# Performance work log

Measured on AMD Instinct MI355X. Metric: run time of the kernel, lower is better.

## Reference

```python
import jax, jax.numpy as jnp
import numpy as np

B, T, V, WD = 32, 2048, 50000, 300        # batch, max_doc_len, batch vocab, word_dim
P, L, ND = 150, 7, 2                      # total patterns, max_pattern_length, num_diags
BIAS_SCALE = 1.0
ZERO = -100.0                             # max-plus semiring zero (repo: neg_infinity = -100*ones)
# end state per pattern = pattern_length - 1, for pattern_specs {5:50, 6:50, 7:50}
END_STATES = np.concatenate([np.full(50, 4), np.full(50, 5), np.full(50, 6)]).astype(np.int32)


def setup_inputs() -> dict:
    key = jax.random.key(0)
    ks = jax.random.split(key, 10)
    diags = jax.random.normal(ks[0], (P * ND * L, WD), jnp.float32)
    diags = diags / jnp.linalg.norm(diags, axis=1, keepdims=True)  # normalize() in __init__
    return {
        "embeddings_matrix": jax.random.normal(ks[1], (WD, V), jnp.float32),
        "diags": diags,
        "bias": jax.random.normal(ks[2], (P * ND * L, 1), jnp.float32),
        "epsilon": jax.random.normal(ks[3], (P, L - 1), jnp.float32),
        "mlp_w0": jax.random.normal(ks[4], (P, 100), jnp.float32) * 0.1,
        "mlp_b0": jnp.zeros((100,), jnp.float32),
        "mlp_w1": jax.random.normal(ks[5], (100, 2), jnp.float32) * 0.1,
        "mlp_b1": jnp.zeros((2,), jnp.float32),
        "docs": jax.random.randint(ks[6], (B, T), 0, V),
        "doc_lens": jax.random.randint(ks[7], (B,), 5, T + 1),
    }


def reference(embeddings_matrix, diags, bias, epsilon, mlp_w0, mlp_b0, mlp_w1, mlp_b1, docs, doc_lens):
    # Max-plus semiring: from_float = identity, times = +, plus = max, one = 0, zero = -100.
    # Transition scores for every token in the batch vocabulary: [V, P*ND*L]
    trans = (diags @ embeddings_matrix + BIAS_SCALE * bias).T
    # Gather per doc token, reshape, time-major: [T, B, P, ND, L]
    tm = trans[docs].reshape(B, T, P, ND, L).transpose(1, 0, 2, 3, 4)

    end_states = jnp.asarray(END_STATES)               # [P]
    active = jnp.arange(T)[:, None] < doc_lens[None, :]  # [T, B]

    zero_pad = jnp.full((B, P, 1), ZERO, trans.dtype)
    restart_pad = jnp.zeros((B, P, 1), trans.dtype)      # semiring one
    hid0 = jnp.full((B, P, L), ZERO, trans.dtype).at[:, :, 0].set(0.0)
    scores0 = jnp.full((B, P), ZERO, trans.dtype)
    eps_val = epsilon                                    # epsilon_scale = semiring one (=0) -> identity

    def step(carry, xs):
        hid, sc = carry
        tmat, act = xs  # tmat: [B, P, ND, L], act: [B]
        # epsilon transitions (shift by one state, additive in max-plus)
        after_eps = jnp.maximum(hid, jnp.concatenate([zero_pad, hid[:, :, :-1] + eps_val], axis=2))
        # main-path transitions (diag index -1), with restart padding at state 0
        main = jnp.concatenate([restart_pad, after_eps[:, :, :-1] + tmat[:, :, -1, :-1]], axis=2)
        # self loops (diag index 0); self_loop_scale = semiring one = 0
        self_loop = hid + tmat[:, :, 0, :]
        hid = jnp.maximum(main, self_loop)
        end_vals = jnp.take_along_axis(hid, end_states[None, :, None], axis=2)[:, :, 0]  # [B, P]
        sc = jnp.where(act[:, None], jnp.maximum(sc, end_vals), sc)
        return (hid, sc), None

    (_, scores), _ = jax.lax.scan(step, (hid0, scores0), (tm, active))
    # MLP head: Linear -> relu -> Linear
    h = scores @ mlp_w0 + mlp_b0
    return jax.nn.relu(h) @ mlp_w1 + mlp_b1
```

## Files before the change

kernel.cpp:

```cpp
#include <hip/hip_runtime.h>
#include <stdint.h>

#define B_   32
#define T_   2048
#define V_   50000
#define WD_  300
#define P_   150
#define KP   320
#define MP   2112
#define MB2  2176
#define NPAD2 50176
#define VT_  391
#define MT_  17
#define NWG3 6664
#define NEGC (-1.0e30f)

#define WS_DIAGSB      32112640u
#define WS_TRANS_BIG   54067200u
#define WS_TRANS_SMALL 33505280u
#define WS_AUX_BIG     265267200u
#define WS_AUX_SMALL   244705280u
#define AUX_BYTES      864260u
#define WS_NEED_BIG    (WS_AUX_BIG + AUX_BYTES)
#define WS_NEED_SMALL  (WS_AUX_SMALL + AUX_BYTES)

typedef __attribute__((ext_vector_type(8))) short bf16x8;
typedef __attribute__((ext_vector_type(4))) float f32x4;

#define GLOAD_LDS16(gp, lp) __builtin_amdgcn_global_load_lds( \
    (__attribute__((address_space(1))) void*)(gp), \
    (__attribute__((address_space(3))) void*)(lp), 16, 0, 0)

__device__ __forceinline__ unsigned short f2bf(float f){
  unsigned u = __builtin_bit_cast(unsigned, f);
  u = u + 0x7fffu + ((u >> 16) & 1u);
  return (unsigned short)(u >> 16);
}
__device__ __forceinline__ float bf_lo(unsigned u){ return __builtin_bit_cast(float, u << 16); }
__device__ __forceinline__ float bf_hi(unsigned u){ return __builtin_bit_cast(float, u & 0xffff0000u); }

__global__ __launch_bounds__(256) void k_transpose_emb(const float* __restrict__ emb,
                                                       unsigned short* __restrict__ embT){
  __shared__ float tile[32][65];
  int v0 = blockIdx.x * 64, k0 = blockIdx.y * 32;
  int tid = threadIdx.x;
  #pragma unroll
  for (int it = 0; it < 8; ++it){
    int idx = it * 256 + tid;
    int kk = idx >> 6, vv = idx & 63;
    int k = k0 + kk, v = v0 + vv;
    float val = 0.f;
    if (k < WD_ && v < V_) val = emb[(size_t)k * V_ + v];
    tile[kk][vv] = val;
  }
  __syncthreads();
  int row = tid >> 2, c = tid & 3;
  unsigned short e[8];
  #pragma unroll
  for (int i = 0; i < 8; ++i) e[i] = f2bf(tile[c*8 + i][row]);
  uint4 pk;
  pk.x = (unsigned)e[0] | ((unsigned)e[1] << 16);
  pk.y = (unsigned)e[2] | ((unsigned)e[3] << 16);
  pk.z = (unsigned)e[4] | ((unsigned)e[5] << 16);
  pk.w = (unsigned)e[6] | ((unsigned)e[7] << 16);
  *(uint4*)&embT[(size_t)(v0 + row) * KP + k0 + c*8] = pk;
}

__global__ __launch_bounds__(256) void k_conv_diags(const float* __restrict__ diags,
                                                    unsigned short* __restrict__ diagsB){
  int gid = blockIdx.x * 256 + threadIdx.x;
  int m = gid / 80;
  int k4 = (gid % 80) * 4;
  unsigned short e[4];
  #pragma unroll
  for (int i = 0; i < 4; ++i){
    int k = k4 + i;
    float v = (m < 2100 && k < WD_) ? diags[m * WD_ + k] : 0.f;
    e[i] = f2bf(v);
  }
  uint2 pk;
  pk.x = (unsigned)e[0] | ((unsigned)e[1] << 16);
  pk.y = (unsigned)e[2] | ((unsigned)e[3] << 16);
  *(uint2*)&diagsB[(size_t)m * KP + k4] = pk;
}

__global__ __launch_bounds__(256) void k_zero(int* __restrict__ used, int* __restrict__ counter){
  int i = blockIdx.x * 256 + threadIdx.x;
  if (i < NPAD2) used[i] = 0;
  if (i == 0) *counter = 0;
}
__global__ __launch_bounds__(256) void k_mark(const int* __restrict__ docs,
                                              const int* __restrict__ dlens,
                                              int* __restrict__ used){
  int i = blockIdx.x * 256 + threadIdx.x;
  int b = i >> 11, t = i & 2047;
  if (t < dlens[b]) used[docs[i]] = 1;
}
__global__ __launch_bounds__(256) void k_compact(const int* __restrict__ used,
                                                 int* __restrict__ remap,
                                                 int* __restrict__ inv,
                                                 int* __restrict__ counter){
  int v = blockIdx.x * 256 + threadIdx.x;
  if (v >= V_) return;
  if (used[v]){
    int id = atomicAdd(counter, 1);
    remap[v] = id;
    inv[id] = v;
  }
}
__global__ __launch_bounds__(256) void k_docsC(const int* __restrict__ docs,
                                               const int* __restrict__ dlens,
                                               const int* __restrict__ remap,
                                               int* __restrict__ docsC){
  int i = blockIdx.x * 256 + threadIdx.x;
  int b = i >> 11, t = i & 2047;
  docsC[i] = (t < dlens[b]) ? remap[docs[i]] : 0;
}

__global__ __launch_bounds__(256, 4) void k_gemm(const unsigned short* __restrict__ embT,
                                                 const unsigned short* __restrict__ diagsB,
                                                 const float* __restrict__ bias,
                                                 const int* __restrict__ inv,
                                                 const int* __restrict__ nusedp,
                                                 unsigned short* __restrict__ trans){
  __shared__ char smem[33792];
  int nused = *nusedp;
  int orig = blockIdx.x;
  int xcd = orig & 7, idx0 = orig >> 3;
  int vt = (idx0 / MT_) * 8 + xcd;
  int mt = idx0 % MT_;
  int v0 = vt * 128, m0 = mt * 128;
  if (v0 >= nused) return;

  int tid = threadIdx.x;
  int w = tid >> 6, l = tid & 63;
  int wv = w & 1, wm = w >> 1;
  int lrow = l & 15, lq = l >> 4;

  int rA0 = tid >> 2, rA1 = 64 + (tid >> 2);
  size_t ga0 = (size_t)((v0 + rA0 < nused) ? inv[v0 + rA0] : 0) * KP;
  size_t ga1 = (size_t)((v0 + rA1 < nused) ? inv[v0 + rA1] : 0) * KP;

  f32x4 acc[4][4];
  #pragma unroll
  for (int i = 0; i < 4; ++i)
    #pragma unroll
    for (int j = 0; j < 4; ++j)
      acc[i][j] = (f32x4){0.f, 0.f, 0.f, 0.f};

  auto STAGE = [&](int buf, int kt){
    int k0 = kt * 32;
    char* bA = smem + buf * 16384;
    char* bB = bA + 8192;
    int slot = tid & 3;
    {
      int idx = tid;
      int sc = slot ^ ((rA0 >> 1) & 3);
      GLOAD_LDS16(&embT[ga0 + k0 + sc * 8], bA + idx * 16);
      int row = idx >> 2;
      int scB = slot ^ ((row >> 1) & 3);
      GLOAD_LDS16(&diagsB[(size_t)(m0 + row) * KP + k0 + scB * 8], bB + idx * 16);
    }
    {
      int idx = 256 + tid;
      int sc = slot ^ ((rA1 >> 1) & 3);
      GLOAD_LDS16(&embT[ga1 + k0 + sc * 8], bA + idx * 16);
      int row = idx >> 2;
      int scB = slot ^ ((row >> 1) & 3);
      GLOAD_LDS16(&diagsB[(size_t)(m0 + row) * KP + k0 + scB * 8], bB + idx * 16);
    }
  };

  STAGE(0, 0);
  #pragma unroll
  for (int kt = 0; kt < 10; ++kt){
    if (kt < 9){
      STAGE((kt + 1) & 1, kt + 1);
      asm volatile("s_waitcnt vmcnt(4)" ::: "memory");
    } else {
      asm volatile("s_waitcnt vmcnt(0)" ::: "memory");
    }
    __builtin_amdgcn_s_barrier();
    __builtin_amdgcn_sched_barrier(0);
    char* bA = smem + (kt & 1) * 16384;
    char* bB = bA + 8192;
    bf16x8 af[4], bg[4];
    #pragma unroll
    for (int i = 0; i < 4; ++i){
      int row = wv * 64 + i * 16 + lrow;
      af[i] = *(const bf16x8*)(bA + row * 64 + (lq ^ ((row >> 1) & 3)) * 16);
    }
    #pragma unroll
    for (int j = 0; j < 4; ++j){
      int row = wm * 64 + j * 16 + lrow;
      bg[j] = *(const bf16x8*)(bB + row * 64 + (lq ^ ((row >> 1) & 3)) * 16);
    }
    #pragma unroll
    for (int i = 0; i < 4; ++i)
      #pragma unroll
      for (int j = 0; j < 4; ++j)
        acc[i][j] = __builtin_amdgcn_mfma_f32_16x16x32_bf16(af[i], bg[j], acc[i][j], 0, 0, 0);
    __builtin_amdgcn_sched_barrier(0);
    __builtin_amdgcn_s_barrier();
  }

  float bv4[4];
  #pragma unroll
  for (int j = 0; j < 4; ++j){
    int mg = m0 + wm * 64 + j * 16 + lrow;
    bv4[j] = (mg < 2100) ? bias[mg] : 0.f;
  }
  unsigned short* eb = (unsigned short*)smem;
  #pragma unroll
  for (int i = 0; i < 4; ++i)
    #pragma unroll
    for (int j = 0; j < 4; ++j)
      #pragma unroll
      for (int r = 0; r < 4; ++r){
        int row = wv * 64 + i * 16 + lq * 4 + r;
        int col = wm * 64 + j * 16 + lrow;
        eb[row * 132 + col] = f2bf(acc[i][j][r] + bv4[j]);
      }
  __syncthreads();
  #pragma unroll
  for (int it = 0; it < 16; ++it){
    int idx2 = it * 256 + tid;
    int row = idx2 >> 5, chq = idx2 & 31;
    int vg = v0 + row, mg = m0 + chq * 4;
    if (vg < nused && mg < MP){
      uint2 val = *(const uint2*)(smem + row * 264 + chq * 8);
      *(uint2*)&trans[(size_t)vg * MP + mg] = val;
    }
  }
}

template<int CH>
__global__ __launch_bounds__(192) void k_scan(const unsigned short* __restrict__ trans,
                                              const int* __restrict__ docsC,
                                              const int* __restrict__ doc_lens,
                                              const float* __restrict__ epsilon,
                                              float* __restrict__ chunkout){
  constexpr int NCHT = T_ / CH;
  __shared__ int sdocs[CH];
  int b = blockIdx.x / NCHT, ch = blockIdx.x % NCHT;
  int doclen = doc_lens[b];
  int tbase = ch * CH;
  if (tbase >= doclen) return;
  int tid = threadIdx.x;
  if (tid < CH) sdocs[tid] = docsC[b * T_ + tbase + tid];
  __syncthreads();
  int p = tid;
  if (p >= P_) return;
  float eps_r[6];
  #pragma unroll
  for (int i = 0; i < 6; ++i) eps_r[i] = epsilon[p*6 + i];
  int endsel = p / 50;

  float col[7][7], bvec[7], uvec[7], w;
  #pragma unroll
  for (int j = 0; j < 7; ++j)
    #pragma unroll
    for (int l = 0; l < 7; ++l) col[j][l] = (j == l) ? 0.f : NEGC;
  #pragma unroll
  for (int l = 0; l < 7; ++l){ bvec[l] = NEGC; uvec[l] = NEGC; }
  w = NEGC;

  const char* transB = (const char*)trans;

  auto LOADQ = [&](unsigned* q, int s){
    int idx = s < CH - 1 ? s : CH - 1;
    const unsigned* rp = (const unsigned*)(transB + (size_t)sdocs[idx] * (MP*2) + p*28);
    #pragma unroll
    for (int i = 0; i < 7; ++i) q[i] = rp[i];
  };

  auto step = [&](const unsigned* q, bool act){
    float tsf[7], tmn[6];
    tsf[0]=bf_lo(q[0]); tsf[1]=bf_hi(q[0]);
    tsf[2]=bf_lo(q[1]); tsf[3]=bf_hi(q[1]);
    tsf[4]=bf_lo(q[2]); tsf[5]=bf_hi(q[2]);
    tsf[6]=bf_lo(q[3]); tmn[0]=bf_hi(q[3]);
    tmn[1]=bf_lo(q[4]); tmn[2]=bf_hi(q[4]);
    tmn[3]=bf_lo(q[5]); tmn[4]=bf_hi(q[5]);
    tmn[5]=bf_lo(q[6]);
    #pragma unroll
    for (int j = 0; j < 7; ++j){
      #pragma unroll
      for (int l = 6; l >= 1; --l){
        if (l < j) continue;
        if (l == j){ col[j][l] = col[j][l] + tsf[l]; continue; }
        float ae;
        if (l - 1 == j) ae = col[j][l-1];
        else ae = fmaxf(col[j][l-1], col[j][l-2] + eps_r[l-2]);
        col[j][l] = fmaxf(ae + tmn[l-1], col[j][l] + tsf[l]);
      }
      if (j == 0) col[0][0] += tsf[0];
    }
    #pragma unroll
    for (int l = 6; l >= 1; --l){
      float ae;
      if (l == 1) ae = fmaxf(bvec[0], -100.0f);
      else ae = fmaxf(bvec[l-1], bvec[l-2] + eps_r[l-2]);
      bvec[l] = fmaxf(ae + tmn[l-1], bvec[l] + tsf[l]);
    }
    bvec[0] = fmaxf(0.0f, bvec[0] + tsf[0]);
    if (act){
      #pragma unroll
      for (int j = 0; j < 7; ++j){
        float c4 = (j <= 4) ? col[j][4] : NEGC;
        float c5 = (j <= 5) ? col[j][5] : NEGC;
        float c6 = col[j][6];
        float ce = (endsel == 0) ? c4 : ((endsel == 1) ? c5 : c6);
        uvec[j] = fmaxf(uvec[j], ce);
      }
      float be = (endsel == 0) ? bvec[4] : ((endsel == 1) ? bvec[5] : bvec[6]);
      w = fmaxf(w, be);
    }
  };

  unsigned qa0[7], qa1[7], qa2[7], qa3[7];
  unsigned qb0[7], qb1[7], qb2[7], qb3[7];
  LOADQ(qa0, 0); LOADQ(qa1, 1); LOADQ(qa2, 2); LOADQ(qa3, 3);
  for (int s = 0; s < CH; s += 8){
    LOADQ(qb0, s + 4); LOADQ(qb1, s + 5); LOADQ(qb2, s + 6); LOADQ(qb3, s + 7);
    step(qa0, (tbase + s)     < doclen);
    step(qa1, (tbase + s + 1) < doclen);
    step(qa2, (tbase + s + 2) < doclen);
    step(qa3, (tbase + s + 3) < doclen);
    LOADQ(qa0, s + 8); LOADQ(qa1, s + 9); LOADQ(qa2, s + 10); LOADQ(qa3, s + 11);
    step(qb0, (tbase + s + 4) < doclen);
    step(qb1, (tbase + s + 5) < doclen);
    step(qb2, (tbase + s + 6) < doclen);
    step(qb3, (tbase + s + 7) < doclen);
  }

  float out[44];
  int idx = 0;
  #pragma unroll
  for (int j = 0; j < 7; ++j)
    #pragma unroll
    for (int l = j; l < 7; ++l) out[idx++] = col[j][l];
  #pragma unroll
  for (int l = 0; l < 7; ++l) out[28 + l] = bvec[l];
  #pragma unroll
  for (int l = 0; l < 7; ++l) out[35 + l] = uvec[l];
  out[42] = w; out[43] = 0.f;
  float* dst = chunkout + ((size_t)(b * NCHT + ch) * P_ + p) * 44;
  #pragma unroll
  for (int i = 0; i < 11; ++i){
    float4 t2 = make_float4(out[4*i], out[4*i+1], out[4*i+2], out[4*i+3]);
    ((float4*)dst)[i] = t2;
  }
}

__global__ __launch_bounds__(192) void k_combine_mlp(const float* __restrict__ chunkout,
                                                     const int* __restrict__ doc_lens,
                                                     const float* __restrict__ w0,
                                                     const float* __restrict__ b0,
                                                     const float* __restrict__ w1,
                                                     const float* __restrict__ b1,
                                                     float* __restrict__ out,
                                                     int nch, int chsz){
  __shared__ float ssc[P_];
  __shared__ float sh[100];
  int b = blockIdx.x, tid = threadIdx.x;
  if (tid < P_){
    int p = tid;
    int doclen = doc_lens[b];
    int nact = (doclen + chsz - 1) / chsz;
    if (nact > nch) nact = nch;
    float h[7] = {0.f, -100.f, -100.f, -100.f, -100.f, -100.f, -100.f};
    float sc = -100.f;
    for (int ch = 0; ch < nact; ++ch){
      const float* rec = chunkout + ((size_t)(b * nch + ch) * P_ + p) * 44;
      float r[44];
      #pragma unroll
      for (int i = 0; i < 11; ++i){
        float4 t = ((const float4*)rec)[i];
        r[4*i] = t.x; r[4*i+1] = t.y; r[4*i+2] = t.z; r[4*i+3] = t.w;
      }
      #pragma unroll
      for (int j = 0; j < 7; ++j) sc = fmaxf(sc, r[35 + j] + h[j]);
      sc = fmaxf(sc, r[42]);
      constexpr int off[7] = {0, 7, 13, 18, 22, 25, 27};
      float nh[7];
      #pragma unroll
      for (int l = 0; l < 7; ++l){
        float v = r[28 + l];
        #pragma unroll
        for (int j = 0; j < 7; ++j){
          if (j <= l) v = fmaxf(v, r[off[j] + (l - j)] + h[j]);
        }
        nh[l] = v;
      }
      #pragma unroll
      for (int l = 0; l < 7; ++l) h[l] = nh[l];
    }
    ssc[p] = sc;
  }
  __syncthreads();
  if (tid < 100){
    float a = b0[tid];
    for (int pp = 0; pp < P_; ++pp) a += ssc[pp] * w0[pp * 100 + tid];
    sh[tid] = fmaxf(a, 0.f);
  }
  __syncthreads();
  if (tid < 2){
    float o = b1[tid];
    for (int j = 0; j < 100; ++j) o += sh[j] * w1[j * 2 + tid];
    out[b * 2 + tid] = o;
  }
}

extern "C" void kernel_launch(void* const* d_in, const int* in_sizes, int n_in,
                              void* d_out, int out_size, void* d_ws, size_t ws_size,
                              hipStream_t stream){
  const float* emb   = (const float*)d_in[0];
  const float* diags = (const float*)d_in[1];
  const float* bias  = (const float*)d_in[2];
  const float* eps   = (const float*)d_in[3];
  const float* w0    = (const float*)d_in[4];
  const float* b0    = (const float*)d_in[5];
  const float* w1    = (const float*)d_in[6];
  const float* b1    = (const float*)d_in[7];
  const int* docs    = (const int*)d_in[8];
  const int* dlens   = (const int*)d_in[9];

  if (ws_size < (size_t)WS_NEED_SMALL) return;
  bool big = ws_size >= (size_t)WS_NEED_BIG;

  char* ws = (char*)d_ws;
  unsigned short* embT   = (unsigned short*)(ws);
  unsigned short* diagsB = (unsigned short*)(ws + WS_DIAGSB);
  unsigned short* trans  = (unsigned short*)(ws + (big ? WS_TRANS_BIG : WS_TRANS_SMALL));
  char* aux              = ws + (big ? WS_AUX_BIG : WS_AUX_SMALL);
  int* used    = (int*)(aux);
  int* remap   = (int*)(aux + 200704u);
  int* inv     = (int*)(aux + 401408u);
  int* docsC   = (int*)(aux + 602112u);
  int* counter = (int*)(aux + 864256u);
  float* chunkout = (float*)(ws);
  float* outp = (float*)d_out;

  k_transpose_emb<<<dim3(NPAD2/64, KP/32), 256, 0, stream>>>(emb, embT);
  k_conv_diags<<<(MB2*80 + 255)/256, 256, 0, stream>>>(diags, diagsB);
  k_zero<<<NPAD2/256, 256, 0, stream>>>(used, counter);
  k_mark<<<B_*T_/256, 256, 0, stream>>>(docs, dlens, used);
  k_compact<<<(V_ + 255)/256, 256, 0, stream>>>(used, remap, inv, counter);
  k_docsC<<<B_*T_/256, 256, 0, stream>>>(docs, dlens, remap, docsC);
  k_gemm<<<NWG3, 256, 0, stream>>>(embT, diagsB, bias, inv, counter, trans);
  if (big){
    k_scan<32><<<B_ * 64, 192, 0, stream>>>(trans, docsC, dlens, eps, chunkout);
    k_combine_mlp<<<B_, 192, 0, stream>>>(chunkout, dlens, w0, b0, w1, b1, outp, 64, 32);
  } else {
    k_scan<64><<<B_ * 32, 192, 0, stream>>>(trans, docsC, dlens, eps, chunkout);
    k_combine_mlp<<<B_, 192, 0, stream>>>(chunkout, dlens, w0, b0, w1, b1, outp, 32, 64);
  }
}
```

Before: 181.7 us.

## Split chunked scan state columns across two workgroups per chunk

Each chunk's scan is split into two workgroups. One tracks start-state columns 0-2 of the max-plus transfer matrix and the other tracks columns 3-6 plus the from-start vector, which doubles the grid and roughly halves per-thread register state and arithmetic. The aim is more occupancy and parallelism in the latency-bound scan. In exchange, both halves reload the same transition rows, and the output is written as scalar stores to disjoint fields instead of packed float4 stores.

```diff
diff --git a/kernel.cpp b/kernel.cpp
--- a/kernel.cpp
+++ b/kernel.cpp
@@ -234,38 +234,20 @@
   }
 }
 
-template<int CH>
-__global__ __launch_bounds__(192) void k_scan(const unsigned short* __restrict__ trans,
-                                              const int* __restrict__ docsC,
-                                              const int* __restrict__ doc_lens,
-                                              const float* __restrict__ epsilon,
-                                              float* __restrict__ chunkout){
-  constexpr int NCHT = T_ / CH;
-  __shared__ int sdocs[CH];
-  int b = blockIdx.x / NCHT, ch = blockIdx.x % NCHT;
-  int doclen = doc_lens[b];
-  int tbase = ch * CH;
-  if (tbase >= doclen) return;
-  int tid = threadIdx.x;
-  if (tid < CH) sdocs[tid] = docsC[b * T_ + tbase + tid];
-  __syncthreads();
-  int p = tid;
-  if (p >= P_) return;
-  float eps_r[6];
-  #pragma unroll
-  for (int i = 0; i < 6; ++i) eps_r[i] = epsilon[p*6 + i];
-  int endsel = p / 50;
-
+template<int CH, int J0, int J1, bool DOB>
+__device__ __forceinline__ void scan_body(const char* __restrict__ transB,
+                                          const int* __restrict__ sdocs,
+                                          int tbase, int doclen,
+                                          const float* eps_r, int endsel, int p,
+                                          float* __restrict__ dst){
   float col[7][7], bvec[7], uvec[7], w;
   #pragma unroll
-  for (int j = 0; j < 7; ++j)
+  for (int j = J0; j < J1; ++j)
     #pragma unroll
     for (int l = 0; l < 7; ++l) col[j][l] = (j == l) ? 0.f : NEGC;
   #pragma unroll
   for (int l = 0; l < 7; ++l){ bvec[l] = NEGC; uvec[l] = NEGC; }
   w = NEGC;
-
-  const char* transB = (const char*)trans;
 
   auto LOADQ = [&](unsigned* q, int s){
     int idx = s < CH - 1 ? s : CH - 1;
@@ -284,7 +266,7 @@
     tmn[3]=bf_lo(q[5]); tmn[4]=bf_hi(q[5]);
     tmn[5]=bf_lo(q[6]);
     #pragma unroll
-    for (int j = 0; j < 7; ++j){
+    for (int j = J0; j < J1; ++j){
       #pragma unroll
       for (int l = 6; l >= 1; --l){
         if (l < j) continue;
@@ -296,25 +278,29 @@
       }
       if (j == 0) col[0][0] += tsf[0];
     }
-    #pragma unroll
-    for (int l = 6; l >= 1; --l){
-      float ae;
-      if (l == 1) ae = fmaxf(bvec[0], -100.0f);
-      else ae = fmaxf(bvec[l-1], bvec[l-2] + eps_r[l-2]);
-      bvec[l] = fmaxf(ae + tmn[l-1], bvec[l] + tsf[l]);
-    }
-    bvec[0] = fmaxf(0.0f, bvec[0] + tsf[0]);
+    if constexpr (DOB){
+      #pragma unroll
+      for (int l = 6; l >= 1; --l){
+        float ae;
+        if (l == 1) ae = fmaxf(bvec[0], -100.0f);
+        else ae = fmaxf(bvec[l-1], bvec[l-2] + eps_r[l-2]);
+        bvec[l] = fmaxf(ae + tmn[l-1], bvec[l] + tsf[l]);
+      }
+      bvec[0] = fmaxf(0.0f, bvec[0] + tsf[0]);
+    }
     if (act){
       #pragma unroll
-      for (int j = 0; j < 7; ++j){
+      for (int j = J0; j < J1; ++j){
         float c4 = (j <= 4) ? col[j][4] : NEGC;
         float c5 = (j <= 5) ? col[j][5] : NEGC;
         float c6 = col[j][6];
         float ce = (endsel == 0) ? c4 : ((endsel == 1) ? c5 : c6);
         uvec[j] = fmaxf(uvec[j], ce);
       }
-      float be = (endsel == 0) ? bvec[4] : ((endsel == 1) ? bvec[5] : bvec[6]);
-      w = fmaxf(w, be);
+      if constexpr (DOB){
+        float be = (endsel == 0) ? bvec[4] : ((endsel == 1) ? bvec[5] : bvec[6]);
+        w = fmaxf(w, be);
+      }
     }
   };
 
@@ -334,23 +320,52 @@
     step(qb3, (tbase + s + 7) < doclen);
   }
 
-  float out[44];
-  int idx = 0;
-  #pragma unroll
-  for (int j = 0; j < 7; ++j)
-    #pragma unroll
-    for (int l = j; l < 7; ++l) out[idx++] = col[j][l];
-  #pragma unroll
-  for (int l = 0; l < 7; ++l) out[28 + l] = bvec[l];
-  #pragma unroll
-  for (int l = 0; l < 7; ++l) out[35 + l] = uvec[l];
-  out[42] = w; out[43] = 0.f;
+  constexpr int off[7] = {0, 7, 13, 18, 22, 25, 27};
+  #pragma unroll
+  for (int j = J0; j < J1; ++j)
+    #pragma unroll
+    for (int l = j; l < 7; ++l) dst[off[j] + (l - j)] = col[j][l];
+  if constexpr (DOB){
+    #pragma unroll
+    for (int l = 0; l < 7; ++l) dst[28 + l] = bvec[l];
+  }
+  #pragma unroll
+  for (int j = J0; j < J1; ++j) dst[35 + j] = uvec[j];
+  if constexpr (DOB) dst[42] = w;
+}
+
+template<int CH>
+__global__ __launch_bounds__(192) void k_scan(const unsigned short* __restrict__ trans,
+                                              const int* __restrict__ docsC,
+                                              const int* __restrict__ doc_lens,
+                                              const float* __restrict__ epsilon,
+                                              float* __restrict__ chunkout){
+  constexpr int NCHT = T_ / CH;
+  __shared__ int sdocs[CH];
+  int raw = blockIdx.x;
+  int part = raw & 1;
+  int cid = raw >> 1;
+  int b = cid / NCHT, ch = cid % NCHT;
+  int doclen = doc_lens[b];
+  int tbase = ch * CH;
+  if (tbase >= doclen) return;
+  int tid = threadIdx.x;
+  if (tid < CH) sdocs[tid] = docsC[b * T_ + tbase + tid];
+  __syncthreads();
+  int p = tid;
+  if (p >= P_) return;
+  float eps_r[6];
+  #pragma unroll
+  for (int i = 0; i < 6; ++i) eps_r[i] = epsilon[p*6 + i];
+  int endsel = p / 50;
+
+  const char* transB = (const char*)trans;
   float* dst = chunkout + ((size_t)(b * NCHT + ch) * P_ + p) * 44;
-  #pragma unroll
-  for (int i = 0; i < 11; ++i){
-    float4 t2 = make_float4(out[4*i], out[4*i+1], out[4*i+2], out[4*i+3]);
-    ((float4*)dst)[i] = t2;
-  }
+
+  if (part == 0)
+    scan_body<CH, 0, 3, false>(transB, sdocs, tbase, doclen, eps_r, endsel, p, dst);
+  else
+    scan_body<CH, 3, 7, true >(transB, sdocs, tbase, doclen, eps_r, endsel, p, dst);
 }
 
 __global__ __launch_bounds__(192) void k_combine_mlp(const float* __restrict__ chunkout,
@@ -450,10 +465,10 @@
   k_docsC<<<B_*T_/256, 256, 0, stream>>>(docs, dlens, remap, docsC);
   k_gemm<<<NWG3, 256, 0, stream>>>(embT, diagsB, bias, inv, counter, trans);
   if (big){
-    k_scan<32><<<B_ * 64, 192, 0, stream>>>(trans, docsC, dlens, eps, chunkout);
+    k_scan<32><<<B_ * 64 * 2, 192, 0, stream>>>(trans, docsC, dlens, eps, chunkout);
     k_combine_mlp<<<B_, 192, 0, stream>>>(chunkout, dlens, w0, b0, w1, b1, outp, 64, 32);
   } else {
-    k_scan<64><<<B_ * 32, 192, 0, stream>>>(trans, docsC, dlens, eps, chunkout);
+    k_scan<64><<<B_ * 32 * 2, 192, 0, stream>>>(trans, docsC, dlens, eps, chunkout);
     k_combine_mlp<<<B_, 192, 0, stream>>>(chunkout, dlens, w0, b0, w1, b1, outp, 32, 64);
   }
 }
```

New measurement: 195.9 us. +7.8%, slower.

## Stage gathered trans rows through double-buffered shared memory in scan kernel

Applied to the files above, without the earlier changes.

The scan kernel now loads whole 4224-byte trans rows for groups of four tokens with coalesced uint4 loads from all threads into registers. It writes them into a double-buffered shared-memory tile, and each pattern thread then reads its 28-byte slice from LDS. This replaces the per-thread strided 4-byte global loads with a register-prefetch pipeline, aiming to cut uncoalesced global traffic. In exchange it adds two block barriers per group, about 33KB of LDS, and idle threads beyond P that must stay alive to help with loads.

```diff
diff --git a/kernel.cpp b/kernel.cpp
--- a/kernel.cpp
+++ b/kernel.cpp
@@ -241,7 +241,9 @@
                                               const float* __restrict__ epsilon,
                                               float* __restrict__ chunkout){
   constexpr int NCHT = T_ / CH;
+  constexpr int NG = CH / 4;
   __shared__ int sdocs[CH];
+  __shared__ char rows[2][4][4224];
   int b = blockIdx.x / NCHT, ch = blockIdx.x % NCHT;
   int doclen = doc_lens[b];
   int tbase = ch * CH;
@@ -250,11 +252,14 @@
   if (tid < CH) sdocs[tid] = docsC[b * T_ + tbase + tid];
   __syncthreads();
   int p = tid;
-  if (p >= P_) return;
-  float eps_r[6];
-  #pragma unroll
-  for (int i = 0; i < 6; ++i) eps_r[i] = epsilon[p*6 + i];
-  int endsel = p / 50;
+  bool act_p = p < P_;
+  float eps_r[6] = {0,0,0,0,0,0};
+  int endsel = 0;
+  if (act_p){
+    #pragma unroll
+    for (int i = 0; i < 6; ++i) eps_r[i] = epsilon[p*6 + i];
+    endsel = p / 50;
+  }
 
   float col[7][7], bvec[7], uvec[7], w;
   #pragma unroll
@@ -267,14 +272,31 @@
 
   const char* transB = (const char*)trans;
 
-  auto LOADQ = [&](unsigned* q, int s){
-    int idx = s < CH - 1 ? s : CH - 1;
-    const unsigned* rp = (const unsigned*)(transB + (size_t)sdocs[idx] * (MP*2) + p*28);
-    #pragma unroll
-    for (int i = 0; i < 7; ++i) q[i] = rp[i];
+  uint4 rg[4][2];
+  #pragma unroll
+  for (int r = 0; r < 4; ++r){ rg[r][0] = make_uint4(0,0,0,0); rg[r][1] = make_uint4(0,0,0,0); }
+
+  auto LOADG = [&](int g){
+    #pragma unroll
+    for (int r = 0; r < 4; ++r){
+      const uint4* src = (const uint4*)(transB + (size_t)sdocs[g*4 + r] * (MP*2));
+      rg[r][0] = src[tid];
+      if (tid < 72) rg[r][1] = src[192 + tid];
+    }
   };
-
-  auto step = [&](const unsigned* q, bool act){
+  auto WRITEG = [&](int buf){
+    #pragma unroll
+    for (int r = 0; r < 4; ++r){
+      uint4* dst = (uint4*)rows[buf][r];
+      dst[tid] = rg[r][0];
+      if (tid < 72) dst[192 + tid] = rg[r][1];
+    }
+  };
+
+  auto stepL = [&](const char* rp, bool act){
+    unsigned q[7];
+    #pragma unroll
+    for (int i = 0; i < 7; ++i) q[i] = *(const unsigned*)(rp + 4*i);
     float tsf[7], tmn[6];
     tsf[0]=bf_lo(q[0]); tsf[1]=bf_hi(q[0]);
     tsf[2]=bf_lo(q[1]); tsf[3]=bf_hi(q[1]);
@@ -318,38 +340,37 @@
     }
   };
 
-  unsigned qa0[7], qa1[7], qa2[7], qa3[7];
-  unsigned qb0[7], qb1[7], qb2[7], qb3[7];
-  LOADQ(qa0, 0); LOADQ(qa1, 1); LOADQ(qa2, 2); LOADQ(qa3, 3);
-  for (int s = 0; s < CH; s += 8){
-    LOADQ(qb0, s + 4); LOADQ(qb1, s + 5); LOADQ(qb2, s + 6); LOADQ(qb3, s + 7);
-    step(qa0, (tbase + s)     < doclen);
-    step(qa1, (tbase + s + 1) < doclen);
-    step(qa2, (tbase + s + 2) < doclen);
-    step(qa3, (tbase + s + 3) < doclen);
-    LOADQ(qa0, s + 8); LOADQ(qa1, s + 9); LOADQ(qa2, s + 10); LOADQ(qa3, s + 11);
-    step(qb0, (tbase + s + 4) < doclen);
-    step(qb1, (tbase + s + 5) < doclen);
-    step(qb2, (tbase + s + 6) < doclen);
-    step(qb3, (tbase + s + 7) < doclen);
-  }
-
-  float out[44];
-  int idx = 0;
-  #pragma unroll
-  for (int j = 0; j < 7; ++j)
-    #pragma unroll
-    for (int l = j; l < 7; ++l) out[idx++] = col[j][l];
-  #pragma unroll
-  for (int l = 0; l < 7; ++l) out[28 + l] = bvec[l];
-  #pragma unroll
-  for (int l = 0; l < 7; ++l) out[35 + l] = uvec[l];
-  out[42] = w; out[43] = 0.f;
-  float* dst = chunkout + ((size_t)(b * NCHT + ch) * P_ + p) * 44;
-  #pragma unroll
-  for (int i = 0; i < 11; ++i){
-    float4 t2 = make_float4(out[4*i], out[4*i+1], out[4*i+2], out[4*i+3]);
-    ((float4*)dst)[i] = t2;
+  LOADG(0); WRITEG(0); __syncthreads();
+  for (int g = 0; g < NG; ++g){
+    if (g + 1 < NG) LOADG(g + 1);
+    if (act_p){
+      #pragma unroll
+      for (int r = 0; r < 4; ++r)
+        stepL(&rows[g & 1][r][p * 28], (tbase + g*4 + r) < doclen);
+    }
+    __syncthreads();
+    if (g + 1 < NG) WRITEG((g + 1) & 1);
+    __syncthreads();
+  }
+
+  if (act_p){
+    float out[44];
+    int idx = 0;
+    #pragma unroll
+    for (int j = 0; j < 7; ++j)
+      #pragma unroll
+      for (int l = j; l < 7; ++l) out[idx++] = col[j][l];
+    #pragma unroll
+    for (int l = 0; l < 7; ++l) out[28 + l] = bvec[l];
+    #pragma unroll
+    for (int l = 0; l < 7; ++l) out[35 + l] = uvec[l];
+    out[42] = w; out[43] = 0.f;
+    float* dst = chunkout + ((size_t)(b * NCHT + ch) * P_ + p) * 44;
+    #pragma unroll
+    for (int i = 0; i < 11; ++i){
+      float4 t2 = make_float4(out[4*i], out[4*i+1], out[4*i+2], out[4*i+3]);
+      ((float4*)dst)[i] = t2;
+    }
   }
 }
 
```

New measurement: 199.8 us. +10.0%, slower.
